# Kernel tuning notes

Measured on AMD Instinct MI355X. Metric: run time of the kernel, lower is better.

Reference implementation:

```python
import jax, jax.numpy as jnp
import numpy as np

B, L, NUM_AA, E, H = 128, 2048, 20, 16, 128

def _mlp(x, W1, b1, W2, b2, W3, b3):
    h = jax.nn.relu(x @ W1 + b1)
    h = jax.nn.relu(h @ W2 + b2)
    return h @ W3 + b3

def _mlp_params(key, in_dim):
    k1, k2, k3 = jax.random.split(key, 3)
    W1 = jax.random.normal(k1, (in_dim, H), jnp.float32) / np.sqrt(in_dim)
    W2 = jax.random.normal(k2, (H, H), jnp.float32) / np.sqrt(H)
    W3 = jax.random.normal(k3, (H, 1), jnp.float32) / np.sqrt(H)
    return W1, jnp.zeros((H,), jnp.float32), W2, jnp.zeros((H,), jnp.float32), W3, jnp.zeros((1,), jnp.float32)

def setup_inputs() -> dict:
    key = jax.random.key(0)
    kR, ks, ke, kl, kt, kp = jax.random.split(key, 6)
    inp = {
        'R': jax.random.normal(kR, (B, L, 3), jnp.float32) * 3.8,  # ~CA-CA scale
        'seq': jax.random.randint(ks, (B, L), 0, NUM_AA),
        'emb': jax.random.normal(ke, (NUM_AA, E), jnp.float32),
    }
    for pref, k, d in (('fl', kl, 1 + 2 * E), ('ft', kt, 1 + 3 * E), ('fp', kp, 2 + 4 * E)):
        W1, b1, W2, b2, W3, b3 = _mlp_params(k, d)
        inp.update({f'{pref}_W1': W1, f'{pref}_b1': b1, f'{pref}_W2': W2, f'{pref}_b2': b2, f'{pref}_W3': W3, f'{pref}_b3': b3})
    return inp

def _energy(R, e, fl, ft, fp):
    d = R[:, 1:, :] - R[:, :-1, :]                      # [B,L-1,3] bond vectors
    lengths = jnp.linalg.norm(d, axis=-1)               # [B,L-1]
    x_l = jnp.concatenate([lengths[..., None], e[:, :-1, :], e[:, 1:, :]], axis=-1)
    E_l = _mlp(x_l, *fl)[..., 0].sum(axis=1)
    # bond angles at atom i+1 between (R[i]-R[i+1]) and (R[i+2]-R[i+1])
    u, v = -d[:, :-1, :], d[:, 1:, :]                   # [B,L-2,3]
    cos_t = jnp.sum(u * v, axis=-1) / (jnp.linalg.norm(u, axis=-1) * jnp.linalg.norm(v, axis=-1))
    theta_in = jnp.clip(cos_t, -1.0, 1.0)               # use_cos_theta=True -> cos(arccos(clip))
    x_t = jnp.concatenate([theta_in[..., None], e[:, :-2, :], e[:, 1:-1, :], e[:, 2:, :]], axis=-1)
    E_t = _mlp(x_t, *ft)[..., 0].sum(axis=1)
    # torsions over quadruples
    b1, b2, b3 = d[:, :-2, :], d[:, 1:-1, :], d[:, 2:, :]
    n1 = jnp.cross(b1, b2)
    n2 = jnp.cross(b2, b3)
    b2u = b2 / jnp.linalg.norm(b2, axis=-1, keepdims=True)
    m1 = jnp.cross(n1, b2u)
    phi = jnp.arctan2(jnp.sum(m1 * n2, axis=-1), jnp.sum(n1 * n2, axis=-1))  # [B,L-3]
    sc = jnp.stack([jnp.sin(phi), jnp.cos(phi)], axis=-1)                    # [B,L-3,2]
    x_p = jnp.concatenate([sc, e[:, :-3, :], e[:, 1:-2, :], e[:, 2:-1, :], e[:, 3:, :]], axis=-1)
    E_p = _mlp(x_p, *fp)[..., 0].sum(axis=1)
    return E_l + E_t + E_p

def reference(R, seq, emb,
              fl_W1, fl_b1, fl_W2, fl_b2, fl_W3, fl_b3,
              ft_W1, ft_b1, ft_W2, ft_b2, ft_W3, ft_b3,
              fp_W1, fp_b1, fp_W2, fp_b2, fp_W3, fp_b3):
    e = emb[seq]                                        # [B,L,E]
    return _energy(R, e,
                   (fl_W1, fl_b1, fl_W2, fl_b2, fl_W3, fl_b3),
                   (ft_W1, ft_b1, ft_W2, ft_b2, ft_W3, ft_b3),
                   (fp_W1, fp_b1, fp_W2, fp_b2, fp_W3, fp_b3))
```

## Files before the change

kernel.cpp:

```cpp
#include <hip/hip_runtime.h>


typedef short bf16x8 __attribute__((ext_vector_type(8)));
typedef float f32x4  __attribute__((ext_vector_type(4)));

constexpr int Lc  = 2048;
constexpr int SHs = 136;

union FragU { uint4 u; bf16x8 v; };

__device__ __forceinline__ unsigned short f2bf(float f) {
    union { float f; unsigned u; } v; v.f = f;
    unsigned u = v.u;
    u = u + 0x7FFFu + ((u >> 16) & 1u);
    return (unsigned short)(u >> 16);
}

__device__ __forceinline__ unsigned pkbf(float a, float b) {
    unsigned ua = __float_as_uint(a) + 0x8000u;
    unsigned ub = __float_as_uint(b) + 0x8000u;
    return __builtin_amdgcn_perm(ub, ua, 0x07060302u);
}

__global__ __launch_bounds__(256)
void prep_kernel(const float* __restrict__ W1_0, const float* __restrict__ b1_0,
                 const float* __restrict__ W1_1, const float* __restrict__ b1_1,
                 const float* __restrict__ W1_2, const float* __restrict__ b1_2,
                 const float* __restrict__ W2_0, const float* __restrict__ W2_1,
                 const float* __restrict__ W2_2,
                 const float* __restrict__ emb, char* __restrict__ ws,
                 float* __restrict__ out)
{
    const int tid = blockIdx.x * 256 + threadIdx.x;
    const int np  = gridDim.x * 256;
    if (blockIdx.x == 0 && threadIdx.x < 128) out[threadIdx.x] = 0.0f;

    unsigned short* d2 = (unsigned short*)ws;
    for (int o = tid; o < 3 * 16384; o += np) {
        int t = o >> 14, r = o & 16383, col = r >> 7, k = r & 127;
        const float* W2 = (t == 0) ? W2_0 : (t == 1) ? W2_1 : W2_2;
        d2[o] = f2bf(W2[k * 128 + col]);
    }
    unsigned short* d1 = (unsigned short*)(ws + 98304);
    for (int o = tid; o < 3 * 12288; o += np) {
        int t = o / 12288, r = o - t * 12288, hid = r / 96, k = r - hid * 96;
        const int NE16 = (t == 0) ? 32 : (t == 1) ? 48 : 64;
        const int NG   = (t == 2) ? 2 : 1;
        const float* W1 = (t == 0) ? W1_0 : (t == 1) ? W1_1 : W1_2;
        const float* b1 = (t == 0) ? b1_0 : (t == 1) ? b1_1 : b1_2;
        float v = 0.0f;
        if (k >= 16) {
            int j = k - 16;
            if (j < NE16) v = W1[(NG + j) * 128 + hid];
        } else if (k == 4) v = b1[hid];
        else if (t == 0 && k == 0) v = W1_0[hid];
        else if (t == 1 && k == 1) v = W1_1[hid];
        else if (t == 2 && k == 2) v = W1_2[hid];
        else if (t == 2 && k == 3) v = W1_2[128 + hid];
        d1[o] = f2bf(v);
    }
    unsigned short* eb = (unsigned short*)(ws + 172032);
    for (int i = tid; i < 320; i += np) eb[i] = f2bf(emb[i]);
}

struct SMem {
    unsigned short H1s[128 * SHs];
    float  Rbuf[393];
    uint2  geomh[128];
    int    seqb[132];
    unsigned short ebuf[320];
    float  part[4];
};

template<int TYPE>
__device__ __forceinline__ void body(
    SMem& sm, const float* __restrict__ R, const int* __restrict__ seq,
    const char* __restrict__ ws,
    const float* __restrict__ b2, const float* __restrict__ w3,
    const float* __restrict__ b3, float* __restrict__ out)
{
    constexpr int NEMB  = (TYPE == 0) ? 2 : (TYPE == 1) ? 3 : 4;
    constexpr int KS    = (TYPE == 2) ? 3 : 2;
    constexpr int ROWSB = Lc - 1 - TYPE;

    const int tid = threadIdx.x;
    const int b   = blockIdx.y;
    const int i0  = blockIdx.x * 128;
    const int lane = tid & 63, wv = tid >> 6;
    const int q = lane >> 4, c = lane & 15;

    const unsigned short* w1t = (const unsigned short*)(ws + 98304 + TYPE * 24576);
    const unsigned short* w2t = (const unsigned short*)(ws + TYPE * 32768);

    for (int t = tid; t < 393; t += 256) {
        int lr = t / 3, comp = t - lr * 3;
        int row = min(i0 + lr, Lc - 1);
        sm.Rbuf[t] = R[((size_t)b * Lc + row) * 3 + comp];
    }
    for (int t = tid; t < 131; t += 256)
        sm.seqb[t] = seq[b * Lc + min(i0 + t, Lc - 1)];
    {
        const uint4* se = (const uint4*)(ws + 172032);
        for (int t = tid; t < 40; t += 256) ((uint4*)sm.ebuf)[t] = se[t];
    }
    __syncthreads();

    if (tid < 128) {
        const float* p0 = &sm.Rbuf[tid * 3];
        float ax = p0[3] - p0[0], ay = p0[4] - p0[1], az = p0[5] - p0[2];
        float bx = p0[6] - p0[3], by = p0[7] - p0[4], bz = p0[8] - p0[5];
        float cx = p0[9] - p0[6], cy = p0[10] - p0[7], cz = p0[11] - p0[8];
        float na2 = ax * ax + ay * ay + az * az;
        float len = sqrtf(na2);
        float nb2 = bx * bx + by * by + bz * bz;
        float duv = -(ax * bx + ay * by + az * bz);
        float cost = fminf(fmaxf(duv / sqrtf(na2 * nb2), -1.0f), 1.0f);
        float n1x = ay * bz - az * by, n1y = az * bx - ax * bz, n1z = ax * by - ay * bx;
        float n2x = by * cz - bz * cy, n2y = bz * cx - bx * cz, n2z = bx * cy - by * cx;
        float binv = 1.0f / sqrtf(nb2);
        float ux = bx * binv, uy = by * binv, uz = bz * binv;
        float m1x = n1y * uz - n1z * uy, m1y = n1z * ux - n1x * uz, m1z = n1x * uy - n1y * ux;
        float yv = m1x * n2x + m1y * n2y + m1z * n2z;
        float xv = n1x * n2x + n1y * n2y + n1z * n2z;
        float inv = 1.0f / sqrtf(xv * xv + yv * yv);
        sm.geomh[tid] = make_uint2(pkbf(len, cost), pkbf(yv * inv, xv * inv));
    }
    __syncthreads();

    FragU A1[2][KS];
#pragma unroll
    for (int mt = 0; mt < 2; ++mt)
#pragma unroll
        for (int ks = 0; ks < KS; ++ks)
            A1[mt][ks].u = *(const uint4*)&w1t[(wv * 32 + mt * 16 + c) * 96 + ks * 32 + q * 8];

    f32x4 acc1[2][8];
#pragma unroll
    for (int mt = 0; mt < 2; ++mt)
#pragma unroll
        for (int nt = 0; nt < 8; ++nt)
            acc1[mt][nt] = (f32x4){0.f, 0.f, 0.f, 0.f};

#pragma unroll
    for (int ks = 0; ks < KS; ++ks) {
        const int k0 = ks * 32 + q * 8;
        const int j = (k0 - 16) >> 4, off = (k0 - 16) & 15;
#pragma unroll
        for (int nt = 0; nt < 8; ++nt) {
            const int m = nt * 16 + c;
            FragU bb;
            if (ks == 0 && q == 0) {
                uint2 g = sm.geomh[m];
                bb.u = make_uint4(g.x, g.y, 0x00003F80u, 0u);
            } else if (k0 >= 16 && j < NEMB) {
                bb.u = *(const uint4*)&sm.ebuf[sm.seqb[m + j] * 16 + off];
            } else {
                bb.u = make_uint4(0u, 0u, 0u, 0u);
            }
            acc1[0][nt] = __builtin_amdgcn_mfma_f32_16x16x32_bf16(A1[0][ks].v, bb.v, acc1[0][nt], 0, 0, 0);
            acc1[1][nt] = __builtin_amdgcn_mfma_f32_16x16x32_bf16(A1[1][ks].v, bb.v, acc1[1][nt], 0, 0, 0);
        }
    }

    const f32x4 z4 = (f32x4){0.f, 0.f, 0.f, 0.f};
#pragma unroll
    for (int mt = 0; mt < 2; ++mt)
#pragma unroll
        for (int nt = 0; nt < 8; ++nt) {
            f32x4 v = __builtin_elementwise_max(acc1[mt][nt], z4);
            uint2 pk;
            pk.x = pkbf(v[0], v[1]);
            pk.y = pkbf(v[2], v[3]);
            *(uint2*)&sm.H1s[(nt * 16 + c) * SHs + wv * 32 + mt * 16 + q * 4] = pk;
        }

    FragU B2[2][4];
#pragma unroll
    for (int nt = 0; nt < 2; ++nt)
#pragma unroll
        for (int ks = 0; ks < 4; ++ks)
            B2[nt][ks].u = *(const uint4*)&w2t[(wv * 32 + nt * 16 + c) * 128 + ks * 32 + q * 8];
    float b2v[2], w3v[2];
#pragma unroll
    for (int nt = 0; nt < 2; ++nt) {
        int col2 = wv * 32 + nt * 16 + c;
        b2v[nt] = b2[col2]; w3v[nt] = w3[col2];
    }
    __syncthreads();

    f32x4 acc2[8][2];
#pragma unroll
    for (int mt = 0; mt < 8; ++mt)
#pragma unroll
        for (int nt = 0; nt < 2; ++nt)
            acc2[mt][nt] = (f32x4){0.f, 0.f, 0.f, 0.f};
#pragma unroll
    for (int ks = 0; ks < 4; ++ks)
#pragma unroll
        for (int mt = 0; mt < 8; ++mt) {
            bf16x8 aa = *(const bf16x8*)&sm.H1s[(mt * 16 + c) * SHs + ks * 32 + q * 8];
            acc2[mt][0] = __builtin_amdgcn_mfma_f32_16x16x32_bf16(aa, B2[0][ks].v, acc2[mt][0], 0, 0, 0);
            acc2[mt][1] = __builtin_amdgcn_mfma_f32_16x16x32_bf16(aa, B2[1][ks].v, acc2[mt][1], 0, 0, 0);
        }

    f32x4 p4 = z4;
#pragma unroll
    for (int mt = 0; mt < 8; ++mt) {
        int mbase = mt * 16 + q * 4;
        if (i0 + mbase + 3 < ROWSB) {
#pragma unroll
            for (int nt = 0; nt < 2; ++nt) {
                f32x4 v = acc2[mt][nt] + b2v[nt];
                v = __builtin_elementwise_max(v, z4);
                p4 += v * w3v[nt];
            }
        } else {
#pragma unroll
            for (int rg = 0; rg < 4; ++rg)
                if (i0 + mbase + rg < ROWSB) {
                    p4[rg] += fmaxf(acc2[mt][0][rg] + b2v[0], 0.f) * w3v[0];
                    p4[rg] += fmaxf(acc2[mt][1][rg] + b2v[1], 0.f) * w3v[1];
                }
        }
    }
    float p = p4[0] + p4[1] + p4[2] + p4[3];
#pragma unroll
    for (int off = 32; off > 0; off >>= 1)
        p += __shfl_down(p, off);
    if (lane == 0) sm.part[wv] = p;
    __syncthreads();
    if (tid == 0) {
        int vc = min(ROWSB - i0, 128);
        atomicAdd(&out[b], sm.part[0] + sm.part[1] + sm.part[2] + sm.part[3]
                           + b3[0] * (float)vc);
    }
}

__global__ __launch_bounds__(256, 4)
void energy_kernel(const float* __restrict__ R, const int* __restrict__ seq,
                   const char* __restrict__ ws,
                   const float* b2_0, const float* b2_1, const float* b2_2,
                   const float* w3_0, const float* w3_1, const float* w3_2,
                   const float* b3_0, const float* b3_1, const float* b3_2,
                   float* __restrict__ out)
{
    __shared__ SMem sm;
    if (blockIdx.z == 0)
        body<0>(sm, R, seq, ws, b2_0, w3_0, b3_0, out);
    else if (blockIdx.z == 1)
        body<1>(sm, R, seq, ws, b2_1, w3_1, b3_1, out);
    else
        body<2>(sm, R, seq, ws, b2_2, w3_2, b3_2, out);
}

extern "C" void kernel_launch(void* const* d_in, const int* in_sizes, int n_in,
                              void* d_out, int out_size, void* d_ws, size_t ws_size,
                              hipStream_t stream) {
    const float* R   = (const float*)d_in[0];
    const int*   seq = (const int*)d_in[1];
    const float* emb = (const float*)d_in[2];
    float* out = (float*)d_out;
    char*  ws  = (char*)d_ws;

    prep_kernel<<<dim3(96), dim3(256), 0, stream>>>(
        (const float*)d_in[3],  (const float*)d_in[4],
        (const float*)d_in[9],  (const float*)d_in[10],
        (const float*)d_in[15], (const float*)d_in[16],
        (const float*)d_in[5],  (const float*)d_in[11], (const float*)d_in[17],
        emb, ws, out);

    dim3 grid(16, 128, 3), block(256);
    energy_kernel<<<grid, block, 0, stream>>>(
        R, seq, ws,
        (const float*)d_in[6],  (const float*)d_in[12], (const float*)d_in[18],
        (const float*)d_in[7],  (const float*)d_in[13], (const float*)d_in[19],
        (const float*)d_in[8],  (const float*)d_in[14], (const float*)d_in[20],
        out);
}
```

Before: 167.7 us.

## Fuse three MLP types into one block and process rows in halves

Each block now computes all three MLP energies (bond, angle, torsion) for its 128-residue tile, so the staging of R and seq, the geometry computation, and the atomic add happen once per tile instead of three times. Each MLP is evaluated in two 64-row halves, which halves the layer-1 shared-memory buffer and the accumulator register arrays. The grid shrinks from 3x to 1x along z. In exchange, each block performs six serialized passes with extra barriers, and there are fewer blocks to hide latency.

```diff
diff --git a/kernel.cpp b/kernel.cpp
--- a/kernel.cpp
+++ b/kernel.cpp
@@ -64,7 +64,7 @@
 }
 
 struct SMem {
-    unsigned short H1s[128 * SHs];
+    unsigned short H1s[64 * SHs];
     float  Rbuf[393];
     uint2  geomh[128];
     int    seqb[132];
@@ -72,25 +72,131 @@
     float  part[4];
 };
 
-template<int TYPE>
-__device__ __forceinline__ void body(
-    SMem& sm, const float* __restrict__ R, const int* __restrict__ seq,
-    const char* __restrict__ ws,
+template<int TYPE, int H>
+__device__ __forceinline__ void half_pass(
+    SMem& sm, const char* __restrict__ ws,
     const float* __restrict__ b2, const float* __restrict__ w3,
-    const float* __restrict__ b3, float* __restrict__ out)
+    int i0, int wv, int q, int c, f32x4& p4)
 {
     constexpr int NEMB  = (TYPE == 0) ? 2 : (TYPE == 1) ? 3 : 4;
     constexpr int KS    = (TYPE == 2) ? 3 : 2;
     constexpr int ROWSB = Lc - 1 - TYPE;
 
+    const unsigned short* w1t = (const unsigned short*)(ws + 98304 + TYPE * 24576);
+    const unsigned short* w2t = (const unsigned short*)(ws + TYPE * 32768);
+
+    FragU A1[2][3];
+#pragma unroll
+    for (int mt = 0; mt < 2; ++mt)
+#pragma unroll
+        for (int ks = 0; ks < KS; ++ks)
+            A1[mt][ks].u = *(const uint4*)&w1t[(wv * 32 + mt * 16 + c) * 96 + ks * 32 + q * 8];
+
+    f32x4 acc1[2][4];
+#pragma unroll
+    for (int mt = 0; mt < 2; ++mt)
+#pragma unroll
+        for (int nt = 0; nt < 4; ++nt)
+            acc1[mt][nt] = (f32x4){0.f, 0.f, 0.f, 0.f};
+
+#pragma unroll
+    for (int ks = 0; ks < KS; ++ks) {
+        const int k0 = ks * 32 + q * 8;
+        const int j = (k0 - 16) >> 4, off = (k0 - 16) & 15;
+#pragma unroll
+        for (int nt = 0; nt < 4; ++nt) {
+            const int m = H * 64 + nt * 16 + c;
+            FragU bb;
+            if (ks == 0 && q == 0) {
+                uint2 g = sm.geomh[m];
+                bb.u = make_uint4(g.x, g.y, 0x00003F80u, 0u);
+            } else if (k0 >= 16 && j < NEMB) {
+                bb.u = *(const uint4*)&sm.ebuf[sm.seqb[m + j] * 16 + off];
+            } else {
+                bb.u = make_uint4(0u, 0u, 0u, 0u);
+            }
+            acc1[0][nt] = __builtin_amdgcn_mfma_f32_16x16x32_bf16(A1[0][ks].v, bb.v, acc1[0][nt], 0, 0, 0);
+            acc1[1][nt] = __builtin_amdgcn_mfma_f32_16x16x32_bf16(A1[1][ks].v, bb.v, acc1[1][nt], 0, 0, 0);
+        }
+    }
+
+    const f32x4 z4 = (f32x4){0.f, 0.f, 0.f, 0.f};
+#pragma unroll
+    for (int mt = 0; mt < 2; ++mt)
+#pragma unroll
+        for (int nt = 0; nt < 4; ++nt) {
+            f32x4 v = __builtin_elementwise_max(acc1[mt][nt], z4);
+            uint2 pk;
+            pk.x = pkbf(v[0], v[1]);
+            pk.y = pkbf(v[2], v[3]);
+            *(uint2*)&sm.H1s[(nt * 16 + c) * SHs + wv * 32 + mt * 16 + q * 4] = pk;
+        }
+
+    FragU B2[2][4];
+#pragma unroll
+    for (int nt = 0; nt < 2; ++nt)
+#pragma unroll
+        for (int ks = 0; ks < 4; ++ks)
+            B2[nt][ks].u = *(const uint4*)&w2t[(wv * 32 + nt * 16 + c) * 128 + ks * 32 + q * 8];
+    float b2v[2], w3v[2];
+#pragma unroll
+    for (int nt = 0; nt < 2; ++nt) {
+        int col2 = wv * 32 + nt * 16 + c;
+        b2v[nt] = b2[col2]; w3v[nt] = w3[col2];
+    }
+    __syncthreads();
+
+    f32x4 acc2[4][2];
+#pragma unroll
+    for (int mt = 0; mt < 4; ++mt)
+#pragma unroll
+        for (int nt = 0; nt < 2; ++nt)
+            acc2[mt][nt] = (f32x4){0.f, 0.f, 0.f, 0.f};
+#pragma unroll
+    for (int ks = 0; ks < 4; ++ks)
+#pragma unroll
+        for (int mt = 0; mt < 4; ++mt) {
+            bf16x8 aa = *(const bf16x8*)&sm.H1s[(mt * 16 + c) * SHs + ks * 32 + q * 8];
+            acc2[mt][0] = __builtin_amdgcn_mfma_f32_16x16x32_bf16(aa, B2[0][ks].v, acc2[mt][0], 0, 0, 0);
+            acc2[mt][1] = __builtin_amdgcn_mfma_f32_16x16x32_bf16(aa, B2[1][ks].v, acc2[mt][1], 0, 0, 0);
+        }
+
+#pragma unroll
+    for (int mt = 0; mt < 4; ++mt) {
+        int mbase = H * 64 + mt * 16 + q * 4;
+        if (i0 + mbase + 3 < ROWSB) {
+#pragma unroll
+            for (int nt = 0; nt < 2; ++nt) {
+                f32x4 v = acc2[mt][nt] + b2v[nt];
+                v = __builtin_elementwise_max(v, z4);
+                p4 += v * w3v[nt];
+            }
+        } else {
+#pragma unroll
+            for (int rg = 0; rg < 4; ++rg)
+                if (i0 + mbase + rg < ROWSB) {
+                    p4[rg] += fmaxf(acc2[mt][0][rg] + b2v[0], 0.f) * w3v[0];
+                    p4[rg] += fmaxf(acc2[mt][1][rg] + b2v[1], 0.f) * w3v[1];
+                }
+        }
+    }
+    __syncthreads();
+}
+
+__global__ __launch_bounds__(256, 4)
+void energy_kernel(const float* __restrict__ R, const int* __restrict__ seq,
+                   const char* __restrict__ ws,
+                   const float* b2_0, const float* b2_1, const float* b2_2,
+                   const float* w3_0, const float* w3_1, const float* w3_2,
+                   const float* b3_0, const float* b3_1, const float* b3_2,
+                   float* __restrict__ out)
+{
+    __shared__ SMem sm;
     const int tid = threadIdx.x;
     const int b   = blockIdx.y;
     const int i0  = blockIdx.x * 128;
     const int lane = tid & 63, wv = tid >> 6;
     const int q = lane >> 4, c = lane & 15;
-
-    const unsigned short* w1t = (const unsigned short*)(ws + 98304 + TYPE * 24576);
-    const unsigned short* w2t = (const unsigned short*)(ws + TYPE * 32768);
 
     for (int t = tid; t < 393; t += 256) {
         int lr = t / 3, comp = t - lr * 3;
@@ -127,102 +233,14 @@
     }
     __syncthreads();
 
-    FragU A1[2][KS];
-#pragma unroll
-    for (int mt = 0; mt < 2; ++mt)
-#pragma unroll
-        for (int ks = 0; ks < KS; ++ks)
-            A1[mt][ks].u = *(const uint4*)&w1t[(wv * 32 + mt * 16 + c) * 96 + ks * 32 + q * 8];
-
-    f32x4 acc1[2][8];
-#pragma unroll
-    for (int mt = 0; mt < 2; ++mt)
-#pragma unroll
-        for (int nt = 0; nt < 8; ++nt)
-            acc1[mt][nt] = (f32x4){0.f, 0.f, 0.f, 0.f};
-
-#pragma unroll
-    for (int ks = 0; ks < KS; ++ks) {
-        const int k0 = ks * 32 + q * 8;
-        const int j = (k0 - 16) >> 4, off = (k0 - 16) & 15;
-#pragma unroll
-        for (int nt = 0; nt < 8; ++nt) {
-            const int m = nt * 16 + c;
-            FragU bb;
-            if (ks == 0 && q == 0) {
-                uint2 g = sm.geomh[m];
-                bb.u = make_uint4(g.x, g.y, 0x00003F80u, 0u);
-            } else if (k0 >= 16 && j < NEMB) {
-                bb.u = *(const uint4*)&sm.ebuf[sm.seqb[m + j] * 16 + off];
-            } else {
-                bb.u = make_uint4(0u, 0u, 0u, 0u);
-            }
-            acc1[0][nt] = __builtin_amdgcn_mfma_f32_16x16x32_bf16(A1[0][ks].v, bb.v, acc1[0][nt], 0, 0, 0);
-            acc1[1][nt] = __builtin_amdgcn_mfma_f32_16x16x32_bf16(A1[1][ks].v, bb.v, acc1[1][nt], 0, 0, 0);
-        }
-    }
-
-    const f32x4 z4 = (f32x4){0.f, 0.f, 0.f, 0.f};
-#pragma unroll
-    for (int mt = 0; mt < 2; ++mt)
-#pragma unroll
-        for (int nt = 0; nt < 8; ++nt) {
-            f32x4 v = __builtin_elementwise_max(acc1[mt][nt], z4);
-            uint2 pk;
-            pk.x = pkbf(v[0], v[1]);
-            pk.y = pkbf(v[2], v[3]);
-            *(uint2*)&sm.H1s[(nt * 16 + c) * SHs + wv * 32 + mt * 16 + q * 4] = pk;
-        }
-
-    FragU B2[2][4];
-#pragma unroll
-    for (int nt = 0; nt < 2; ++nt)
-#pragma unroll
-        for (int ks = 0; ks < 4; ++ks)
-            B2[nt][ks].u = *(const uint4*)&w2t[(wv * 32 + nt * 16 + c) * 128 + ks * 32 + q * 8];
-    float b2v[2], w3v[2];
-#pragma unroll
-    for (int nt = 0; nt < 2; ++nt) {
-        int col2 = wv * 32 + nt * 16 + c;
-        b2v[nt] = b2[col2]; w3v[nt] = w3[col2];
-    }
-    __syncthreads();
-
-    f32x4 acc2[8][2];
-#pragma unroll
-    for (int mt = 0; mt < 8; ++mt)
-#pragma unroll
-        for (int nt = 0; nt < 2; ++nt)
-            acc2[mt][nt] = (f32x4){0.f, 0.f, 0.f, 0.f};
-#pragma unroll
-    for (int ks = 0; ks < 4; ++ks)
-#pragma unroll
-        for (int mt = 0; mt < 8; ++mt) {
-            bf16x8 aa = *(const bf16x8*)&sm.H1s[(mt * 16 + c) * SHs + ks * 32 + q * 8];
-            acc2[mt][0] = __builtin_amdgcn_mfma_f32_16x16x32_bf16(aa, B2[0][ks].v, acc2[mt][0], 0, 0, 0);
-            acc2[mt][1] = __builtin_amdgcn_mfma_f32_16x16x32_bf16(aa, B2[1][ks].v, acc2[mt][1], 0, 0, 0);
-        }
-
-    f32x4 p4 = z4;
-#pragma unroll
-    for (int mt = 0; mt < 8; ++mt) {
-        int mbase = mt * 16 + q * 4;
-        if (i0 + mbase + 3 < ROWSB) {
-#pragma unroll
-            for (int nt = 0; nt < 2; ++nt) {
-                f32x4 v = acc2[mt][nt] + b2v[nt];
-                v = __builtin_elementwise_max(v, z4);
-                p4 += v * w3v[nt];
-            }
-        } else {
-#pragma unroll
-            for (int rg = 0; rg < 4; ++rg)
-                if (i0 + mbase + rg < ROWSB) {
-                    p4[rg] += fmaxf(acc2[mt][0][rg] + b2v[0], 0.f) * w3v[0];
-                    p4[rg] += fmaxf(acc2[mt][1][rg] + b2v[1], 0.f) * w3v[1];
-                }
-        }
-    }
+    f32x4 p4 = (f32x4){0.f, 0.f, 0.f, 0.f};
+    half_pass<0, 0>(sm, ws, b2_0, w3_0, i0, wv, q, c, p4);
+    half_pass<0, 1>(sm, ws, b2_0, w3_0, i0, wv, q, c, p4);
+    half_pass<1, 0>(sm, ws, b2_1, w3_1, i0, wv, q, c, p4);
+    half_pass<1, 1>(sm, ws, b2_1, w3_1, i0, wv, q, c, p4);
+    half_pass<2, 0>(sm, ws, b2_2, w3_2, i0, wv, q, c, p4);
+    half_pass<2, 1>(sm, ws, b2_2, w3_2, i0, wv, q, c, p4);
+
     float p = p4[0] + p4[1] + p4[2] + p4[3];
 #pragma unroll
     for (int off = 32; off > 0; off >>= 1)
@@ -230,27 +248,12 @@
     if (lane == 0) sm.part[wv] = p;
     __syncthreads();
     if (tid == 0) {
-        int vc = min(ROWSB - i0, 128);
-        atomicAdd(&out[b], sm.part[0] + sm.part[1] + sm.part[2] + sm.part[3]
-                           + b3[0] * (float)vc);
-    }
-}
-
-__global__ __launch_bounds__(256, 4)
-void energy_kernel(const float* __restrict__ R, const int* __restrict__ seq,
-                   const char* __restrict__ ws,
-                   const float* b2_0, const float* b2_1, const float* b2_2,
-                   const float* w3_0, const float* w3_1, const float* w3_2,
-                   const float* b3_0, const float* b3_1, const float* b3_2,
-                   float* __restrict__ out)
-{
-    __shared__ SMem sm;
-    if (blockIdx.z == 0)
-        body<0>(sm, R, seq, ws, b2_0, w3_0, b3_0, out);
-    else if (blockIdx.z == 1)
-        body<1>(sm, R, seq, ws, b2_1, w3_1, b3_1, out);
-    else
-        body<2>(sm, R, seq, ws, b2_2, w3_2, b3_2, out);
+        float tot = sm.part[0] + sm.part[1] + sm.part[2] + sm.part[3];
+        tot += b3_0[0] * (float)min(Lc - 1 - i0, 128);
+        tot += b3_1[0] * (float)min(Lc - 2 - i0, 128);
+        tot += b3_2[0] * (float)min(Lc - 3 - i0, 128);
+        atomicAdd(&out[b], tot);
+    }
 }
 
 extern "C" void kernel_launch(void* const* d_in, const int* in_sizes, int n_in,
@@ -269,7 +272,7 @@
         (const float*)d_in[5],  (const float*)d_in[11], (const float*)d_in[17],
         emb, ws, out);
 
-    dim3 grid(16, 128, 3), block(256);
+    dim3 grid(16, 128), block(256);
     energy_kernel<<<grid, block, 0, stream>>>(
         R, seq, ws,
         (const float*)d_in[6],  (const float*)d_in[12], (const float*)d_in[18],
```

Result: no change. 165.7 us (-1.2%).
